# Optimization experiments

Measured on AMD Instinct MI355X. Metric: run time of the kernel, lower is better.

## Reference

```python
import jax, jax.numpy as jnp
import numpy as np

B, IN, H = 131072, 128, 128


def setup_inputs() -> dict:
    key = jax.random.key(0)
    ks = jax.random.split(key, 8)
    scale_W = 1.0 / np.sqrt(IN + H)
    scale_r = 1.0 / np.sqrt(H)
    return {
        "x": jax.random.normal(ks[0], (B, IN), jnp.float32),
        "h": jax.random.normal(ks[1], (B, H), jnp.float32),
        "c": jax.random.normal(ks[2], (B, H), jnp.float32),
        "n": jax.random.uniform(ks[3], (B, H), jnp.float32, 0.1, 1.0),
        "m": jax.random.normal(ks[4], (B, H), jnp.float32),
        "W": jax.random.normal(ks[5], (IN + H, 4 * H), jnp.float32) * scale_W,
        "r": jax.random.normal(ks[6], (H, 4 * H), jnp.float32) * scale_r,
        "b": jnp.zeros((4 * H,), jnp.float32),
    }


def reference(x, h, c, n, m, W, r, b):
    # fused gate pre-activations: [B, 4H]
    combined = jnp.concatenate((x, h), axis=1)
    gates = combined @ W + h @ r + b
    i_raw, f_raw, z_raw, o_raw = jnp.split(gates, 4, axis=1)
    i = jnp.exp(i_raw)
    f = jax.nn.sigmoid(f_raw)
    z = jnp.tanh(z_raw)
    o = jax.nn.sigmoid(o_raw)
    # log-domain stabilizer (max trick), faithful to source incl. m overwrite
    m_new = jnp.maximum(jnp.log(f) + m, jnp.log(i))
    i_prime = jnp.exp(jnp.log(i) - m_new)
    f_prime = jnp.exp(jnp.log(f) + m_new - m_new)  # == f, as in source
    c_new = f_prime * c + i_prime * z
    n_new = f_prime * n + i_prime
    h_tilde = c_new / n_new
    h_new = o * jnp.tanh(h_tilde)
    return (h_new, c_new, n_new, m_new)
```

## Files before the change

### kernel.cpp

```cpp
#include <hip/hip_runtime.h>
#include <cstdint>

#define NROWS 131072
#define HD    128
#define NDIM  512
#define OUTQ  16777216

using bf16x8 = __attribute__((ext_vector_type(8))) short;
using f32x4  = __attribute__((ext_vector_type(4))) float;

__device__ __forceinline__ uint32_t bf16rne(float f) {
  uint32_t u = __builtin_bit_cast(uint32_t, f);
  return (u + 0x7fffu + ((u >> 16) & 1u)) >> 16;
}

__device__ __forceinline__ float tanhf_fast(float v) {
  float a = __builtin_fabsf(v);
  float e = __expf(-2.0f * a);
  float t = (1.0f - e) * __builtin_amdgcn_rcpf(1.0f + e);
  return v < 0.0f ? -t : t;
}

__device__ __forceinline__ f32x4 ldv(const float* p) {
  return *reinterpret_cast<const f32x4*>(p);
}

#define ASYNC16(g, l)                                                        \
  __builtin_amdgcn_global_load_lds(                                          \
      (const __attribute__((address_space(1))) void*)(g),                    \
      (__attribute__((address_space(3))) void*)(l), 16, 0, 0)

__global__ __launch_bounds__(256) void pack_weights(
    const float* __restrict__ W, const float* __restrict__ r,
    uint16_t* __restrict__ Bp) {
  int idx = blockIdx.x * 256 + threadIdx.x;
  int l  = idx & 63;
  int ts = idx >> 6;
  int s  = ts & 7;
  int t  = ts >> 3;
  int g  = t >> 3;
  int u  = t & 7;
  int t2 = u >> 1;
  int p  = u & 1;
  int m  = l & 15;
  int ncol  = g * 128 + t2 * 32 + ((m >> 2) << 3) + p * 4 + (m & 3);
  int kbase = s * 32 + ((l >> 4) << 3);
  uint32_t w[4];
#pragma unroll
  for (int jj = 0; jj < 4; ++jj) {
    int k0 = kbase + 2 * jj;
    float v0 = W[k0 * NDIM + ncol];
    float v1 = W[(k0 + 1) * NDIM + ncol];
    if (k0 >= 128)     v0 += r[(k0 - 128) * NDIM + ncol];
    if (k0 + 1 >= 128) v1 += r[(k0 + 1 - 128) * NDIM + ncol];
    w[jj] = bf16rne(v0) | (bf16rne(v1) << 16);
  }
  reinterpret_cast<uint4*>(Bp)[idx] = make_uint4(w[0], w[1], w[2], w[3]);
}

__global__ __launch_bounds__(256, 2) void slstm_fused(
    const float* __restrict__ x,  const float* __restrict__ h,
    const float* __restrict__ cs, const float* __restrict__ ns,
    const float* __restrict__ ms, const float* __restrict__ bias,
    const uint16_t* __restrict__ Bp, float* __restrict__ out) {
  __shared__ __align__(16) char smem[65536];
  const int tid  = threadIdx.x;
  const int wave = tid >> 6;
  const int lane = tid & 63;
  const int row0 = blockIdx.x * 64;
  const int l15  = lane & 15;
  const int lg   = lane >> 4;

  const int    myrow = row0 + wave * 16 + l15;
  const size_t rbase = (size_t)myrow * HD;
  const int    jb8   = lg * 8;

  const char* wBytes = (const char*)Bp;
#define DMA_HALFSTEP(u)                                                      \
  {                                                                          \
    const char* gsrc = wBytes + (((size_t)(wave * 8 + (u)) * 8) << 10) + (lane << 4); \
    char* ldst = smem + (((u) & 1) << 15) + (wave << 13);                    \
    _Pragma("unroll")                                                        \
    for (int k = 0; k < 8; ++k)                                              \
      ASYNC16(gsrc + (k << 10), ldst + (k << 10));                           \
  }

  f32x4 cvA = ldv(cs + rbase + jb8), cvHiA = ldv(cs + rbase + jb8 + 4);
  f32x4 nvA = ldv(ns + rbase + jb8), nvHiA = ldv(ns + rbase + jb8 + 4);
  f32x4 mvA = ldv(ms + rbase + jb8), mvHiA = ldv(ms + rbase + jb8 + 4);

  DMA_HALFSTEP(0)

  bf16x8 a[8];
#pragma unroll
  for (int s = 0; s < 8; ++s) {
    const float* src = (s < 4 ? x : h) + rbase + ((s & 3) * 32 + lg * 8);
    f32x4 v0 = ldv(src);
    f32x4 v1 = ldv(src + 4);
    bf16x8 pk;
    pk[0] = (short)bf16rne(v0[0]);
    pk[1] = (short)bf16rne(v0[1]);
    pk[2] = (short)bf16rne(v0[2]);
    pk[3] = (short)bf16rne(v0[3]);
    pk[4] = (short)bf16rne(v1[0]);
    pk[5] = (short)bf16rne(v1[1]);
    pk[6] = (short)bf16rne(v1[2]);
    pk[7] = (short)bf16rne(v1[3]);
    a[s] = pk;
  }

#define MFMA_PHASE(u, AI, AF, AZ, AO)                                        \
  {                                                                          \
    const char* wb = smem + (((u) & 1) << 15);                               \
    _Pragma("unroll")                                                        \
    for (int s = 0; s < 8; ++s) {                                            \
      const int lo = lane << 4;                                              \
      bf16x8 wI = *reinterpret_cast<const bf16x8*>(wb + ((0 * 8 + s) << 10) + lo); \
      bf16x8 wF = *reinterpret_cast<const bf16x8*>(wb + ((1 * 8 + s) << 10) + lo); \
      bf16x8 wZ = *reinterpret_cast<const bf16x8*>(wb + ((2 * 8 + s) << 10) + lo); \
      bf16x8 wO = *reinterpret_cast<const bf16x8*>(wb + ((3 * 8 + s) << 10) + lo); \
      AI = __builtin_amdgcn_mfma_f32_16x16x32_bf16(wI, a[s], AI, 0, 0, 0);   \
      AF = __builtin_amdgcn_mfma_f32_16x16x32_bf16(wF, a[s], AF, 0, 0, 0);   \
      AZ = __builtin_amdgcn_mfma_f32_16x16x32_bf16(wZ, a[s], AZ, 0, 0, 0);   \
      AO = __builtin_amdgcn_mfma_f32_16x16x32_bf16(wO, a[s], AO, 0, 0, 0);   \
    }                                                                        \
  }

#pragma unroll
  for (int t2 = 0; t2 < 4; ++t2) {
    const int u0 = 2 * t2, u1 = u0 + 1;
    const int cb = t2 * 32 + jb8;

    const f32x4 cvLo = cvA,   cvHi = cvHiA;
    const f32x4 nvLo = nvA,   nvHi = nvHiA;
    const f32x4 mvLo = mvA,   mvHi = mvHiA;

    __syncthreads();
    DMA_HALFSTEP(u1)

    f32x4 accI0 = {0,0,0,0}, accF0 = {0,0,0,0}, accZ0 = {0,0,0,0}, accO0 = {0,0,0,0};
    MFMA_PHASE(u0, accI0, accF0, accZ0, accO0)

    __syncthreads();
    if (t2 < 3) DMA_HALFSTEP(u0 + 2)

    const f32x4 bIlo = ldv(bias + cb),        bIhi = ldv(bias + cb + 4);
    const f32x4 bFlo = ldv(bias + 128 + cb),  bFhi = ldv(bias + 128 + cb + 4);
    const f32x4 bZlo = ldv(bias + 256 + cb),  bZhi = ldv(bias + 256 + cb + 4);
    const f32x4 bOlo = ldv(bias + 384 + cb),  bOhi = ldv(bias + 384 + cb + 4);

    f32x4 accI1 = {0,0,0,0}, accF1 = {0,0,0,0}, accZ1 = {0,0,0,0}, accO1 = {0,0,0,0};
    MFMA_PHASE(u1, accI1, accF1, accZ1, accO1)

    if (t2 < 3) {
      const size_t pp = rbase + (t2 + 1) * 32 + jb8;
      cvA = ldv(cs + pp); cvHiA = ldv(cs + pp + 4);
      nvA = ldv(ns + pp); nvHiA = ldv(ns + pp + 4);
      mvA = ldv(ms + pp); mvHiA = ldv(ms + pp + 4);
    }

    f32x4 hnLo, hnHi, cnLo, cnHi, nnLo, nnHi, mnLo, mnHi;
#pragma unroll
    for (int d = 0; d < 8; ++d) {
      const int pp = d >> 2, rr = d & 3;
      const float i_raw = (pp ? accI1[rr] : accI0[rr]) + (pp ? bIhi[rr] : bIlo[rr]);
      const float f_raw = (pp ? accF1[rr] : accF0[rr]) + (pp ? bFhi[rr] : bFlo[rr]);
      const float z_raw = (pp ? accZ1[rr] : accZ0[rr]) + (pp ? bZhi[rr] : bZlo[rr]);
      const float o_raw = (pp ? accO1[rr] : accO0[rr]) + (pp ? bOhi[rr] : bOlo[rr]);
      const float cV = pp ? cvHi[rr] : cvLo[rr];
      const float nV = pp ? nvHi[rr] : nvLo[rr];
      const float mV = pp ? mvHi[rr] : mvLo[rr];
      float ef  = __expf(-f_raw);
      float den = 1.0f + ef;
      float fg  = __builtin_amdgcn_rcpf(den);
      float lgf = -__logf(den);
      float mnv = fmaxf(lgf + mV, i_raw);
      float ip  = __expf(i_raw - mnv);
      float zt  = tanhf_fast(z_raw);
      float og  = __builtin_amdgcn_rcpf(1.0f + __expf(-o_raw));
      float cnv = fg * cV + ip * zt;
      float nnv = fg * nV + ip;
      float hnv = og * tanhf_fast(cnv * __builtin_amdgcn_rcpf(nnv));
      if (pp == 0) { hnLo[rr] = hnv; cnLo[rr] = cnv; nnLo[rr] = nnv; mnLo[rr] = mnv; }
      else         { hnHi[rr] = hnv; cnHi[rr] = cnv; nnHi[rr] = nnv; mnHi[rr] = mnv; }
    }
    const size_t pbase = rbase + cb;
    *reinterpret_cast<f32x4*>(out + pbase)                = hnLo;
    *reinterpret_cast<f32x4*>(out + pbase + 4)            = hnHi;
    *reinterpret_cast<f32x4*>(out + OUTQ + pbase)         = cnLo;
    *reinterpret_cast<f32x4*>(out + OUTQ + pbase + 4)     = cnHi;
    *reinterpret_cast<f32x4*>(out + 2 * OUTQ + pbase)     = nnLo;
    *reinterpret_cast<f32x4*>(out + 2 * OUTQ + pbase + 4) = nnHi;
    *reinterpret_cast<f32x4*>(out + 3 * OUTQ + pbase)     = mnLo;
    *reinterpret_cast<f32x4*>(out + 3 * OUTQ + pbase + 4) = mnHi;
  }
#undef DMA_HALFSTEP
#undef MFMA_PHASE
}

extern "C" void kernel_launch(void* const* d_in, const int* in_sizes, int n_in,
                              void* d_out, int out_size, void* d_ws, size_t ws_size,
                              hipStream_t stream) {
  const float* x = (const float*)d_in[0];
  const float* h = (const float*)d_in[1];
  const float* c = (const float*)d_in[2];
  const float* n = (const float*)d_in[3];
  const float* m = (const float*)d_in[4];
  const float* W = (const float*)d_in[5];
  const float* r = (const float*)d_in[6];
  const float* b = (const float*)d_in[7];
  uint16_t* Bp = (uint16_t*)d_ws;

  pack_weights<<<64, 256, 0, stream>>>(W, r, Bp);
  slstm_fused<<<NROWS / 64, 256, 0, stream>>>(x, h, c, n, m, b, Bp, (float*)d_out);
}
```

Before: 150.1 us.

## Stage outputs through swizzled LDS for coalesced row stores, single-buffer weights

Output tiles (h, c, n, m) are first written to a swizzled LDS staging area, then each wave writes one output tensor with full 128-byte row segments, so global stores are contiguous instead of 32-byte scattered fragments. To make room in LDS, the weight double buffer becomes a single 32 KB buffer. Weight DMA is now serialized with the MFMA phases and extra __syncthreads are added. That removes the overlap between weight loads and compute in exchange for better store coalescing.

```diff
diff --git a/kernel.cpp b/kernel.cpp
--- a/kernel.cpp
+++ b/kernel.cpp
@@ -74,12 +74,13 @@
   const int    myrow = row0 + wave * 16 + l15;
   const size_t rbase = (size_t)myrow * HD;
   const int    jb8   = lg * 8;
+  const int    rl    = wave * 16 + l15;
 
   const char* wBytes = (const char*)Bp;
 #define DMA_HALFSTEP(u)                                                      \
   {                                                                          \
     const char* gsrc = wBytes + (((size_t)(wave * 8 + (u)) * 8) << 10) + (lane << 4); \
-    char* ldst = smem + (((u) & 1) << 15) + (wave << 13);                    \
+    char* ldst = smem + (wave << 13);                                        \
     _Pragma("unroll")                                                        \
     for (int k = 0; k < 8; ++k)                                              \
       ASYNC16(gsrc + (k << 10), ldst + (k << 10));                           \
@@ -109,16 +110,15 @@
     a[s] = pk;
   }
 
-#define MFMA_PHASE(u, AI, AF, AZ, AO)                                        \
+#define MFMA_PHASE(AI, AF, AZ, AO)                                           \
   {                                                                          \
-    const char* wb = smem + (((u) & 1) << 15);                               \
     _Pragma("unroll")                                                        \
     for (int s = 0; s < 8; ++s) {                                            \
       const int lo = lane << 4;                                              \
-      bf16x8 wI = *reinterpret_cast<const bf16x8*>(wb + ((0 * 8 + s) << 10) + lo); \
-      bf16x8 wF = *reinterpret_cast<const bf16x8*>(wb + ((1 * 8 + s) << 10) + lo); \
-      bf16x8 wZ = *reinterpret_cast<const bf16x8*>(wb + ((2 * 8 + s) << 10) + lo); \
-      bf16x8 wO = *reinterpret_cast<const bf16x8*>(wb + ((3 * 8 + s) << 10) + lo); \
+      bf16x8 wI = *reinterpret_cast<const bf16x8*>(smem + ((0 * 8 + s) << 10) + lo); \
+      bf16x8 wF = *reinterpret_cast<const bf16x8*>(smem + ((1 * 8 + s) << 10) + lo); \
+      bf16x8 wZ = *reinterpret_cast<const bf16x8*>(smem + ((2 * 8 + s) << 10) + lo); \
+      bf16x8 wO = *reinterpret_cast<const bf16x8*>(smem + ((3 * 8 + s) << 10) + lo); \
       AI = __builtin_amdgcn_mfma_f32_16x16x32_bf16(wI, a[s], AI, 0, 0, 0);   \
       AF = __builtin_amdgcn_mfma_f32_16x16x32_bf16(wF, a[s], AF, 0, 0, 0);   \
       AZ = __builtin_amdgcn_mfma_f32_16x16x32_bf16(wZ, a[s], AZ, 0, 0, 0);   \
@@ -126,9 +126,10 @@
     }                                                                        \
   }
 
+  char* sbuf = smem + 32768;
+
 #pragma unroll
   for (int t2 = 0; t2 < 4; ++t2) {
-    const int u0 = 2 * t2, u1 = u0 + 1;
     const int cb = t2 * 32 + jb8;
 
     const f32x4 cvLo = cvA,   cvHi = cvHiA;
@@ -136,28 +137,27 @@
     const f32x4 mvLo = mvA,   mvHi = mvHiA;
 
     __syncthreads();
-    DMA_HALFSTEP(u1)
 
     f32x4 accI0 = {0,0,0,0}, accF0 = {0,0,0,0}, accZ0 = {0,0,0,0}, accO0 = {0,0,0,0};
-    MFMA_PHASE(u0, accI0, accF0, accZ0, accO0)
-
-    __syncthreads();
-    if (t2 < 3) DMA_HALFSTEP(u0 + 2)
+    MFMA_PHASE(accI0, accF0, accZ0, accO0)
+
+    __syncthreads();
+    DMA_HALFSTEP(2 * t2 + 1)
+    __syncthreads();
 
     const f32x4 bIlo = ldv(bias + cb),        bIhi = ldv(bias + cb + 4);
     const f32x4 bFlo = ldv(bias + 128 + cb),  bFhi = ldv(bias + 128 + cb + 4);
     const f32x4 bZlo = ldv(bias + 256 + cb),  bZhi = ldv(bias + 256 + cb + 4);
     const f32x4 bOlo = ldv(bias + 384 + cb),  bOhi = ldv(bias + 384 + cb + 4);
-
-    f32x4 accI1 = {0,0,0,0}, accF1 = {0,0,0,0}, accZ1 = {0,0,0,0}, accO1 = {0,0,0,0};
-    MFMA_PHASE(u1, accI1, accF1, accZ1, accO1)
-
     if (t2 < 3) {
       const size_t pp = rbase + (t2 + 1) * 32 + jb8;
       cvA = ldv(cs + pp); cvHiA = ldv(cs + pp + 4);
       nvA = ldv(ns + pp); nvHiA = ldv(ns + pp + 4);
       mvA = ldv(ms + pp); mvHiA = ldv(ms + pp + 4);
     }
+
+    f32x4 accI1 = {0,0,0,0}, accF1 = {0,0,0,0}, accZ1 = {0,0,0,0}, accO1 = {0,0,0,0};
+    MFMA_PHASE(accI1, accF1, accZ1, accO1)
 
     f32x4 hnLo, hnHi, cnLo, cnHi, nnLo, nnHi, mnLo, mnHi;
 #pragma unroll
@@ -184,15 +184,39 @@
       if (pp == 0) { hnLo[rr] = hnv; cnLo[rr] = cnv; nnLo[rr] = nnv; mnLo[rr] = mnv; }
       else         { hnHi[rr] = hnv; cnHi[rr] = cnv; nnHi[rr] = nnv; mnHi[rr] = mnv; }
     }
-    const size_t pbase = rbase + cb;
-    *reinterpret_cast<f32x4*>(out + pbase)                = hnLo;
-    *reinterpret_cast<f32x4*>(out + pbase + 4)            = hnHi;
-    *reinterpret_cast<f32x4*>(out + OUTQ + pbase)         = cnLo;
-    *reinterpret_cast<f32x4*>(out + OUTQ + pbase + 4)     = cnHi;
-    *reinterpret_cast<f32x4*>(out + 2 * OUTQ + pbase)     = nnLo;
-    *reinterpret_cast<f32x4*>(out + 2 * OUTQ + pbase + 4) = nnHi;
-    *reinterpret_cast<f32x4*>(out + 3 * OUTQ + pbase)     = mnLo;
-    *reinterpret_cast<f32x4*>(out + 3 * OUTQ + pbase + 4) = mnHi;
+
+    {
+      const int rb   = rl << 7;
+      const int sw   = rl & 7;
+      const int kLo  = (lg << 1);
+      const int kHi  = (lg << 1) | 1;
+      const int oLo  = rb + (((kLo) ^ sw) << 4);
+      const int oHi  = rb + (((kHi) ^ sw) << 4);
+      *reinterpret_cast<f32x4*>(sbuf + 0 * 8192 + oLo) = hnLo;
+      *reinterpret_cast<f32x4*>(sbuf + 0 * 8192 + oHi) = hnHi;
+      *reinterpret_cast<f32x4*>(sbuf + 1 * 8192 + oLo) = cnLo;
+      *reinterpret_cast<f32x4*>(sbuf + 1 * 8192 + oHi) = cnHi;
+      *reinterpret_cast<f32x4*>(sbuf + 2 * 8192 + oLo) = nnLo;
+      *reinterpret_cast<f32x4*>(sbuf + 2 * 8192 + oHi) = nnHi;
+      *reinterpret_cast<f32x4*>(sbuf + 3 * 8192 + oLo) = mnLo;
+      *reinterpret_cast<f32x4*>(sbuf + 3 * 8192 + oHi) = mnHi;
+    }
+    __syncthreads();
+
+    if (t2 < 3) DMA_HALFSTEP(2 * t2 + 2)
+
+    {
+      float* abase = out + (size_t)wave * OUTQ + (size_t)row0 * HD + t2 * 32;
+      const char* sb = sbuf + (wave << 13);
+#pragma unroll
+      for (int i = 0; i < 8; ++i) {
+        const int r  = i * 8 + (lane >> 3);
+        const int k  = lane & 7;
+        f32x4 v = *reinterpret_cast<const f32x4*>(
+            sb + (r << 7) + (((k ^ (r & 7))) << 4));
+        *reinterpret_cast<f32x4*>(abase + (size_t)r * HD + k * 4) = v;
+      }
+    }
   }
 #undef DMA_HALFSTEP
 #undef MFMA_PHASE
```

Result: no change. 149.3 us (-0.5%).
